# Optimization experiments

Measured on AMD Instinct MI355X. Metric: run time of the kernel, lower is better.

Reference implementation:

```python
import jax, jax.numpy as jnp
import numpy as np
import math

NL = 2
ENC = 64

def _ln(x, g, b):
    m = x.mean(-1, keepdims=True)
    v = ((x - m) ** 2).mean(-1, keepdims=True)
    return (x - m) * jax.lax.rsqrt(v + 1e-5) * g + b

def _sinu(vals):
    half = ENC // 2
    freq = jnp.exp(jnp.arange(half, dtype=vals.dtype) * (-math.log(10000.0) / half))
    a = vals[..., None] * freq
    return jnp.concatenate([jnp.sin(a), jnp.cos(a)], -1)

def _ssm(x, ng, nb, piw, pib, pw, pb, ig, ib):
    # SSMBlock with LinearAttention core: x + proj_out(LN(silu(z)*sigmoid(gate)))
    h = _ln(x, ng, nb)
    zi = h @ piw + pib
    z, gate = jnp.split(zi, 2, axis=-1)
    u = _ln(jax.nn.silu(z) * jax.nn.sigmoid(gate), ig, ib)
    return x + u @ pw + pb

def _fwd(s, attn_maps, km, se_w1, se_b1, se_w2, se_b2,
         f_ng, f_nb, f_piw, f_pib, f_pow, f_pob, f_ig, f_ib,
         b_ng, b_nb, b_piw, b_pib, b_pow, b_pob, b_ig, b_ib,
         mrg_w, mrg_b, nrm_g, nrm_b,
         ffn_ng, ffn_nb, ffn_w1, ffn_b1, ffn_w2, ffn_b2, H, W):
    B, K, D = s.shape
    w = attn_maps / (attn_maps.sum(-1, keepdims=True) + 1e-8)  # [B,K,N]
    gy = jnp.arange(H, dtype=s.dtype) / max(H - 1, 1)
    gx = jnp.arange(W, dtype=s.dtype) / max(W - 1, 1)
    grid_y = jnp.repeat(gy, W)  # [N], meshgrid-ij flattened
    grid_x = jnp.tile(gx, H)
    cy = (w * grid_y).sum(-1)  # [B,K]
    cx = (w * grid_x).sum(-1)
    spread = jnp.sqrt((w * ((grid_y - cy[..., None]) ** 2 + (grid_x - cx[..., None]) ** 2)).sum(-1))
    enc = jnp.concatenate([_sinu(cy), _sinu(cx), spread[..., None]], -1)  # [B,K,129]
    s = s + jax.nn.gelu(enc @ se_w1 + se_b1, approximate=False) @ se_w2 + se_b2
    # spatial order: identical every layer since attn_maps is fixed
    order = jnp.argsort(cy * W + cx, axis=-1)  # [B,K]
    rv = jnp.argsort(order, axis=-1)           # inverse permutation
    for i in range(NL):
        r = s
        so = jnp.take_along_axis(s, order[..., None], axis=1)
        f = _ssm(so, f_ng[i], f_nb[i], f_piw[i], f_pib[i], f_pow[i], f_pob[i], f_ig[i], f_ib[i])
        bb = jnp.flip(_ssm(jnp.flip(so, 1), b_ng[i], b_nb[i], b_piw[i], b_pib[i], b_pow[i], b_pob[i], b_ig[i], b_ib[i]), 1)
        m = jnp.concatenate([f, bb], -1) @ mrg_w[i] + mrg_b[i]
        s = _ln(r + jnp.take_along_axis(m, rv[..., None], axis=1), nrm_g[i], nrm_b[i])
        h = _ln(s, ffn_ng[i], ffn_nb[i])
        s = s + jax.nn.gelu(h @ ffn_w1[i] + ffn_b1[i], approximate=False) @ ffn_w2[i] + ffn_b2[i]
        s = s * km[..., None]
    return s

def setup_inputs() -> dict:
    B, K, D, DI, H, W = 32, 256, 512, 1024, 64, 64
    N = H * W
    ks = iter(jax.random.split(jax.random.key(0), 64))
    def g(shape, sc=0.02):
        return jax.random.normal(next(ks), shape, dtype=jnp.float32) * sc
    inp = {
        's': jax.random.normal(next(ks), (B, K, D), dtype=jnp.float32),
        'attn_maps': jax.random.uniform(next(ks), (B, K, N), dtype=jnp.float32),
        'km': jnp.ones((B, K), jnp.float32),
        'se_w1': g((2 * ENC + 1, D)), 'se_b1': jnp.zeros((D,), jnp.float32),
        'se_w2': g((D, D)), 'se_b2': jnp.zeros((D,), jnp.float32),
    }
    for p in ('f', 'b'):
        inp[p + '_ng'] = jnp.ones((NL, D), jnp.float32)
        inp[p + '_nb'] = jnp.zeros((NL, D), jnp.float32)
        inp[p + '_piw'] = g((NL, D, 2 * DI))
        inp[p + '_pib'] = jnp.zeros((NL, 2 * DI), jnp.float32)
        inp[p + '_pow'] = g((NL, DI, D))
        inp[p + '_pob'] = jnp.zeros((NL, D), jnp.float32)
        inp[p + '_ig'] = jnp.ones((NL, DI), jnp.float32)
        inp[p + '_ib'] = jnp.zeros((NL, DI), jnp.float32)
    inp['mrg_w'] = g((NL, 2 * D, D)); inp['mrg_b'] = jnp.zeros((NL, D), jnp.float32)
    inp['nrm_g'] = jnp.ones((NL, D), jnp.float32); inp['nrm_b'] = jnp.zeros((NL, D), jnp.float32)
    inp['ffn_ng'] = jnp.ones((NL, D), jnp.float32); inp['ffn_nb'] = jnp.zeros((NL, D), jnp.float32)
    inp['ffn_w1'] = g((NL, D, 4 * D)); inp['ffn_b1'] = jnp.zeros((NL, 4 * D), jnp.float32)
    inp['ffn_w2'] = g((NL, 4 * D, D)); inp['ffn_b2'] = jnp.zeros((NL, D), jnp.float32)
    inp['H'] = H
    inp['W'] = W
    return inp

def reference(s, attn_maps, km, se_w1, se_b1, se_w2, se_b2,
              f_ng, f_nb, f_piw, f_pib, f_pow, f_pob, f_ig, f_ib,
              b_ng, b_nb, b_piw, b_pib, b_pow, b_pob, b_ig, b_ib,
              mrg_w, mrg_b, nrm_g, nrm_b,
              ffn_ng, ffn_nb, ffn_w1, ffn_b1, ffn_w2, ffn_b2, H, W):
    return _fwd(s, attn_maps, km, se_w1, se_b1, se_w2, se_b2,
                f_ng, f_nb, f_piw, f_pib, f_pow, f_pob, f_ig, f_ib,
                b_ng, b_nb, b_piw, b_pib, b_pow, b_pob, b_ig, b_ib,
                mrg_w, mrg_b, nrm_g, nrm_b,
                ffn_ng, ffn_nb, ffn_w1, ffn_b1, ffn_w2, ffn_b2, H, W)
```

## Files before the change

### kernel.cpp

```cpp
#include <hip/hip_runtime.h>
#include <cstdint>
#include <cstddef>


typedef unsigned short u16;
typedef __bf16 bf16x8 __attribute__((ext_vector_type(8)));
typedef float f32x4 __attribute__((ext_vector_type(4)));

#define MROWS 8192

__device__ __forceinline__ u16 f2bf(float f){
  unsigned u = __float_as_uint(f);
  u += 0x7FFFu + ((u >> 16) & 1u);
  return (u16)(u >> 16);
}

__device__ __forceinline__ float wred64(float v){
#pragma unroll
  for (int o = 32; o > 0; o >>= 1) v += __shfl_xor(v, o, 64);
  return v;
}

#define GLD16(gp, lp) __builtin_amdgcn_global_load_lds( \
    (const __attribute__((address_space(1))) unsigned int*)(gp), \
    (__attribute__((address_space(3))) unsigned int*)(lp), 16, 0, 0)

__global__ __launch_bounds__(256) void transpose_w(
    const float* __restrict__ in, u16* __restrict__ out,
    int R, int C, int Kpad, int zgate){
  __shared__ float tile[32][33];
  int n0 = blockIdx.x << 5, k0 = blockIdx.y << 5;
  int tx = threadIdx.x & 31, ty = threadIdx.x >> 5;
#pragma unroll
  for (int i = 0; i < 32; i += 8){
    int k = k0 + ty + i, n = n0 + tx;
    int oc = n;
    if (zgate){ int g = n >> 5, sl = n & 31;
      oc = (sl < 16) ? (g << 4) + sl : (C >> 1) + (g << 4) + sl - 16; }
    tile[ty + i][tx] = (k < R) ? in[(size_t)k * C + oc] : 0.f;
  }
  __syncthreads();
#pragma unroll
  for (int i = 0; i < 32; i += 8){
    int n = n0 + ty + i, k = k0 + tx;
    out[(size_t)n * Kpad + k] = f2bf(tile[tx][ty + i]);
  }
}

__global__ __launch_bounds__(256) void perm_bias(
    const float* __restrict__ in, float* __restrict__ out){
  int n = blockIdx.x * 256 + threadIdx.x;
  int g = n >> 5, sl = n & 31;
  out[n] = in[(sl < 16) ? (g << 4) + sl : 1024 + (g << 4) + sl - 16];
}

__global__ __launch_bounds__(256) void stats_enc(
    const float* __restrict__ attn, u16* __restrict__ enc){
  int row = blockIdx.x;
  const float4* a4 = (const float4*)(attn + (size_t)row * 4096);
  int t = threadIdx.x;
  const float inv63 = 1.0f / 63.0f;
  float s0 = 0, sy = 0, sx = 0, sy2 = 0, sx2 = 0;
#pragma unroll
  for (int i = 0; i < 4; ++i){
    int c = t + 256 * i;
    float4 v = a4[c];
    int n = 4 * c;
#pragma unroll
    for (int e = 0; e < 4; ++e){
      float av = (&v.x)[e];
      int nn = n + e;
      float gy = (float)(nn >> 6) * inv63;
      float gx = (float)(nn & 63) * inv63;
      s0 += av; sy += av * gy; sx += av * gx;
      sy2 += av * gy * gy; sx2 += av * gx * gx;
    }
  }
  s0 = wred64(s0); sy = wred64(sy); sx = wred64(sx);
  sy2 = wred64(sy2); sx2 = wred64(sx2);
  __shared__ float red[4][5];
  __shared__ float outv[3];
  int wv = t >> 6, lane = t & 63;
  if (lane == 0){ red[wv][0]=s0; red[wv][1]=sy; red[wv][2]=sx; red[wv][3]=sy2; red[wv][4]=sx2; }
  __syncthreads();
  if (t == 0){
    float S=0, Ay=0, Ax=0, Ay2=0, Ax2=0;
    for (int w = 0; w < 4; ++w){ S+=red[w][0]; Ay+=red[w][1]; Ax+=red[w][2]; Ay2+=red[w][3]; Ax2+=red[w][4]; }
    float denom = S + 1e-8f;
    float cy = Ay / denom, cx = Ax / denom;
    float sp2 = (Ay2 - 2.f*cy*Ay + cy*cy*S + Ax2 - 2.f*cx*Ax + cx*cx*S) / denom;
    outv[0] = cy; outv[1] = cx; outv[2] = sqrtf(fmaxf(sp2, 0.f));
  }
  __syncthreads();
  if (t < 192){
    float cy = outv[0], cx = outv[1];
    float val = 0.f;
    if (t < 128){
      int j = t & 31;
      float fr = expf(-0.28782313662425572f * (float)j);
      float base = (t < 64) ? cy : cx;
      float ang = base * fr;
      val = ((t >> 5) & 1) ? cosf(ang) : sinf(ang);
    } else if (t == 128) val = outv[2];
    enc[(size_t)row * 192 + t] = f2bf(val);
  }
}

__global__ __launch_bounds__(256) void ln_dual(
    const float* __restrict__ x,
    const float* __restrict__ g1, const float* __restrict__ b1,
    const float* __restrict__ g2, const float* __restrict__ b2,
    u16* __restrict__ o1, u16* __restrict__ o2){
  int row = blockIdx.x * 4 + (threadIdx.x >> 6);
  int lane = threadIdx.x & 63, c = lane * 8;
  const float* xr = x + (size_t)row * 512 + c;
  float v[8];
  *(float4*)(v) = *(const float4*)(xr); *(float4*)(v+4) = *(const float4*)(xr+4);
  float s = 0.f;
#pragma unroll
  for (int j = 0; j < 8; ++j) s += v[j];
  float m = wred64(s) * (1.f/512.f);
  float q = 0.f;
#pragma unroll
  for (int j = 0; j < 8; ++j){ float d = v[j]-m; q += d*d; }
  float rstd = rsqrtf(wred64(q)*(1.f/512.f) + 1e-5f);
  float G1[8],B1[8],G2[8],B2[8];
  *(float4*)(G1)=*(const float4*)(g1+c); *(float4*)(G1+4)=*(const float4*)(g1+c+4);
  *(float4*)(B1)=*(const float4*)(b1+c); *(float4*)(B1+4)=*(const float4*)(b1+c+4);
  *(float4*)(G2)=*(const float4*)(g2+c); *(float4*)(G2+4)=*(const float4*)(g2+c+4);
  *(float4*)(B2)=*(const float4*)(b2+c); *(float4*)(B2+4)=*(const float4*)(b2+c+4);
  u16 u1[8] __attribute__((aligned(16)));
  u16 u2[8] __attribute__((aligned(16)));
#pragma unroll
  for (int j = 0; j < 8; ++j){
    float nv = (v[j]-m)*rstd;
    u1[j] = f2bf(nv*G1[j]+B1[j]);
    u2[j] = f2bf(nv*G2[j]+B2[j]);
  }
  *(uint4*)(o1 + (size_t)row*512 + c) = *(const uint4*)u1;
  *(uint4*)(o2 + (size_t)row*512 + c) = *(const uint4*)u2;
}

__global__ __launch_bounds__(256) void ln1024(
    const float* __restrict__ x, const float* __restrict__ g,
    const float* __restrict__ b, u16* __restrict__ o){
  int row = blockIdx.x * 4 + (threadIdx.x >> 6);
  int lane = threadIdx.x & 63, c = lane * 16;
  const float* xr = x + (size_t)row * 1024 + c;
  float v[16];
#pragma unroll
  for (int i = 0; i < 4; ++i) *(float4*)(v + 4*i) = *(const float4*)(xr + 4*i);
  float s = 0.f;
#pragma unroll
  for (int j = 0; j < 16; ++j) s += v[j];
  float m = wred64(s) * (1.f/1024.f);
  float q = 0.f;
#pragma unroll
  for (int j = 0; j < 16; ++j){ float d = v[j]-m; q += d*d; }
  float rstd = rsqrtf(wred64(q)*(1.f/1024.f) + 1e-5f);
  float G[16], B[16];
#pragma unroll
  for (int i = 0; i < 4; ++i){
    *(float4*)(G + 4*i) = *(const float4*)(g + c + 4*i);
    *(float4*)(B + 4*i) = *(const float4*)(b + c + 4*i);
  }
  u16 u[16] __attribute__((aligned(16)));
#pragma unroll
  for (int j = 0; j < 16; ++j) u[j] = f2bf((v[j]-m)*rstd*G[j] + B[j]);
  *(uint4*)(o + (size_t)row*1024 + c)     = *(const uint4*)(u);
  *(uint4*)(o + (size_t)row*1024 + c + 8) = *(const uint4*)(u + 8);
}

__global__ __launch_bounds__(256) void ln_double(
    const float* __restrict__ x,
    const float* __restrict__ ng, const float* __restrict__ nb,
    const float* __restrict__ fg, const float* __restrict__ fbv,
    float* __restrict__ s1, u16* __restrict__ h2){
  int row = blockIdx.x * 4 + (threadIdx.x >> 6);
  int lane = threadIdx.x & 63, c = lane * 8;
  const float* xr = x + (size_t)row * 512 + c;
  float v[8];
  *(float4*)(v) = *(const float4*)(xr); *(float4*)(v+4) = *(const float4*)(xr+4);
  float s = 0.f;
#pragma unroll
  for (int j = 0; j < 8; ++j) s += v[j];
  float m = wred64(s) * (1.f/512.f);
  float q = 0.f;
#pragma unroll
  for (int j = 0; j < 8; ++j){ float d = v[j]-m; q += d*d; }
  float rstd = rsqrtf(wred64(q)*(1.f/512.f) + 1e-5f);
  float NG[8],NB[8],FG[8],FB[8];
  *(float4*)(NG)=*(const float4*)(ng+c); *(float4*)(NG+4)=*(const float4*)(ng+c+4);
  *(float4*)(NB)=*(const float4*)(nb+c); *(float4*)(NB+4)=*(const float4*)(nb+c+4);
  *(float4*)(FG)=*(const float4*)(fg+c); *(float4*)(FG+4)=*(const float4*)(fg+c+4);
  *(float4*)(FB)=*(const float4*)(fbv+c);*(float4*)(FB+4)=*(const float4*)(fbv+c+4);
  float w[8];
#pragma unroll
  for (int j = 0; j < 8; ++j) w[j] = (v[j]-m)*rstd*NG[j] + NB[j];
  *(float4*)(s1 + (size_t)row*512 + c)   = *(const float4*)(w);
  *(float4*)(s1 + (size_t)row*512 + c+4) = *(const float4*)(w+4);
  float s2 = 0.f;
#pragma unroll
  for (int j = 0; j < 8; ++j) s2 += w[j];
  float m2 = wred64(s2) * (1.f/512.f);
  float q2 = 0.f;
#pragma unroll
  for (int j = 0; j < 8; ++j){ float d = w[j]-m2; q2 += d*d; }
  float rstd2 = rsqrtf(wred64(q2)*(1.f/512.f) + 1e-5f);
  u16 u[8] __attribute__((aligned(16)));
#pragma unroll
  for (int j = 0; j < 8; ++j) u[j] = f2bf((w[j]-m2)*rstd2*FG[j] + FB[j]);
  *(uint4*)(h2 + (size_t)row*512 + c) = *(const uint4*)u;
}

template<int EPI>
__global__ __launch_bounds__(256, 2) void gemm_bt(
    const u16* __restrict__ A, const u16* __restrict__ BT,
    const float* __restrict__ bias, const float* __restrict__ res,
    float* __restrict__ outF, u16* __restrict__ outB,
    const float* __restrict__ km,
    int K, int N, int ldo, int coloff){
  __shared__ u16 Asm[128 * 64];
  __shared__ u16 Bsm[128 * 64];
  const int tid = threadIdx.x, wv = tid >> 6, lane = tid & 63;
  const int m0 = blockIdx.y << 7, n0 = blockIdx.x << 7;
  const int wr = wv >> 1, wc = wv & 1;

  const int rload = (wv << 5) + (lane >> 3);
  const int ksrc = ((16 * (lane & 7)) ^ (((lane >> 3) & 7) << 4)) >> 1;
  const u16* gA = A + (size_t)(m0 + rload) * K + ksrc;
  const u16* gB = BT + (size_t)(n0 + rload) * K + ksrc;
  u16* ldsA = Asm + (wv << 11);
  u16* ldsB = Bsm + (wv << 11);

  f32x4 acc[4][4] = {};
  const int cbase = 16 * (lane >> 4);
  const int swz = (lane & 7) << 4;

  for (int kt = 0; kt < K; kt += 64){
#pragma unroll
    for (int it = 0; it < 4; ++it){
      GLD16(gA + (size_t)it * 8 * K + kt, ldsA + it * 512);
      GLD16(gB + (size_t)it * 8 * K + kt, ldsB + it * 512);
    }
    __syncthreads();
#pragma unroll
    for (int ks = 0; ks < 64; ks += 32){
      const int cs = ((2 * ks + cbase) ^ swz) >> 1;
      bf16x8 af[4], bfr[4];
#pragma unroll
      for (int m = 0; m < 4; ++m)
        af[m] = *reinterpret_cast<const bf16x8*>(&Asm[(wr*64 + m*16 + (lane & 15)) * 64 + cs]);
#pragma unroll
      for (int n = 0; n < 4; ++n)
        bfr[n] = *reinterpret_cast<const bf16x8*>(&Bsm[(wc*64 + n*16 + (lane & 15)) * 64 + cs]);
#pragma unroll
      for (int m = 0; m < 4; ++m)
#pragma unroll
        for (int n = 0; n < 4; ++n)
          acc[m][n] = __builtin_amdgcn_mfma_f32_16x16x32_bf16(af[m], bfr[n], acc[m][n], 0, 0, 0);
    }
    __syncthreads();
  }

  const int lr = (lane >> 4) << 2, lc = lane & 15;
#pragma unroll
  for (int m = 0; m < 4; ++m){
    const int grow0 = m0 + wr * 64 + m * 16 + lr;
    if constexpr (EPI == 3){
#pragma unroll
      for (int n = 0; n < 4; n += 2){
        const int zc = n0 + wc * 64 + n * 16 + lc;
        const float bz = bias[zc], bg = bias[zc + 16];
        const int ucol = ((n0 + wc * 64) >> 1) + (n << 3) + lc;
#pragma unroll
        for (int r = 0; r < 4; ++r){
          float z = acc[m][n][r] + bz;
          float g = acc[m][n + 1][r] + bg;
          outF[(size_t)(grow0 + r) * ldo + ucol] =
              (z / (1.f + expf(-z))) * (1.f / (1.f + expf(-g)));
        }
      }
    } else {
#pragma unroll
      for (int n = 0; n < 4; ++n){
        const int col = n0 + wc * 64 + n * 16 + lc;
        const float bv = bias[col];
#pragma unroll
        for (int r = 0; r < 4; ++r){
          const int grow = grow0 + r;
          float v = acc[m][n][r] + bv;
          if constexpr (EPI == 0){
            outB[(size_t)grow * ldo + col] = f2bf(0.5f * v * (1.f + erff(v * 0.70710678118654752f)));
          } else if constexpr (EPI == 1){
            outF[(size_t)grow * ldo + col] = v + res[(size_t)grow * N + col];
          } else if constexpr (EPI == 2){
            outF[(size_t)grow * ldo + col] = (v + res[(size_t)grow * N + col]) * km[grow];
          } else {
            outB[(size_t)grow * ldo + coloff + col] = f2bf(v + res[(size_t)grow * N + col]);
          }
        }
      }
    }
  }
}

extern "C" void kernel_launch(void* const* d_in, const int* in_sizes, int n_in,
                              void* d_out, int out_size, void* d_ws, size_t ws_size,
                              hipStream_t stream){
  (void)in_sizes; (void)n_in; (void)out_size; (void)ws_size;
  const float* s_in   = (const float*)d_in[0];
  const float* attn   = (const float*)d_in[1];
  const float* km     = (const float*)d_in[2];
  const float* se_w1  = (const float*)d_in[3];
  const float* se_b1  = (const float*)d_in[4];
  const float* se_w2  = (const float*)d_in[5];
  const float* se_b2  = (const float*)d_in[6];
  const float* png[2] = {(const float*)d_in[7],  (const float*)d_in[15]};
  const float* pnb[2] = {(const float*)d_in[8],  (const float*)d_in[16]};
  const float* ppiw[2]= {(const float*)d_in[9],  (const float*)d_in[17]};
  const float* ppib[2]= {(const float*)d_in[10], (const float*)d_in[18]};
  const float* ppow[2]= {(const float*)d_in[11], (const float*)d_in[19]};
  const float* ppob[2]= {(const float*)d_in[12], (const float*)d_in[20]};
  const float* pig[2] = {(const float*)d_in[13], (const float*)d_in[21]};
  const float* pibt[2]= {(const float*)d_in[14], (const float*)d_in[22]};
  const float* mrg_w  = (const float*)d_in[23];
  const float* mrg_b  = (const float*)d_in[24];
  const float* nrm_g  = (const float*)d_in[25];
  const float* nrm_b  = (const float*)d_in[26];
  const float* ffn_ng = (const float*)d_in[27];
  const float* ffn_nb = (const float*)d_in[28];
  const float* ffn_w1 = (const float*)d_in[29];
  const float* ffn_b1 = (const float*)d_in[30];
  const float* ffn_w2 = (const float*)d_in[31];
  const float* ffn_b2 = (const float*)d_in[32];
  float* out = (float*)d_out;

  char* ws = (char*)d_ws;
  size_t off = 0;
  auto alloc = [&](size_t bytes)->char*{
    char* p = ws + off; off += (bytes + 255) & ~(size_t)255; return p; };

  u16* w_sew1 = (u16*)alloc(512 * 192 * 2);
  u16* w_sew2 = (u16*)alloc(512 * 512 * 2);
  u16* w_piw[2][2]; u16* w_pow[2][2]; float* pibp[2][2];
  for (int d = 0; d < 2; ++d)
    for (int i = 0; i < 2; ++i){
      w_piw[d][i] = (u16*)alloc(2048 * 512 * 2);
      w_pow[d][i] = (u16*)alloc(512 * 1024 * 2);
      pibp[d][i]  = (float*)alloc(2048 * 4);
    }
  u16* w_mrg[2]; u16* w_ffn1[2]; u16* w_ffn2[2];
  for (int i = 0; i < 2; ++i){
    w_mrg[i]  = (u16*)alloc(512 * 1024 * 2);
    w_ffn1[i] = (u16*)alloc(2048 * 512 * 2);
    w_ffn2[i] = (u16*)alloc(512 * 2048 * 2);
  }
  u16*   enc  = (u16*)alloc((size_t)MROWS * 192 * 2);
  u16*   t1h2 = (u16*)alloc((size_t)MROWS * 512 * 2);
  float* sc   = (float*)alloc((size_t)MROWS * 512 * 4);
  u16*   hf   = (u16*)alloc((size_t)MROWS * 512 * 2);
  u16*   hb   = (u16*)alloc((size_t)MROWS * 512 * 2);
  char*  big  = alloc((size_t)MROWS * 1024 * 4);
  float* upre = (float*)big;
  float* r2   = (float*)big;
  u16*   t2   = (u16*)big;
  u16*   ubf  = (u16*)alloc((size_t)MROWS * 1024 * 2);
  u16*   fbuf = (u16*)alloc((size_t)MROWS * 1024 * 2);
  float* s1   = (float*)alloc((size_t)MROWS * 512 * 4);

  transpose_w<<<dim3(16, 6),  256, 0, stream>>>(se_w1, w_sew1, 129, 512, 192, 0);
  transpose_w<<<dim3(16, 16), 256, 0, stream>>>(se_w2, w_sew2, 512, 512, 512, 0);
  for (int d = 0; d < 2; ++d)
    for (int i = 0; i < 2; ++i){
      transpose_w<<<dim3(64, 16), 256, 0, stream>>>(ppiw[d] + (size_t)i*512*2048, w_piw[d][i], 512, 2048, 512, 1);
      transpose_w<<<dim3(16, 32), 256, 0, stream>>>(ppow[d] + (size_t)i*1024*512, w_pow[d][i], 1024, 512, 1024, 0);
      perm_bias<<<8, 256, 0, stream>>>(ppib[d] + (size_t)i*2048, pibp[d][i]);
    }
  for (int i = 0; i < 2; ++i){
    transpose_w<<<dim3(16, 32), 256, 0, stream>>>(mrg_w  + (size_t)i*1024*512, w_mrg[i],  1024, 512, 1024, 0);
    transpose_w<<<dim3(64, 16), 256, 0, stream>>>(ffn_w1 + (size_t)i*512*2048, w_ffn1[i], 512, 2048, 512, 0);
    transpose_w<<<dim3(16, 64), 256, 0, stream>>>(ffn_w2 + (size_t)i*2048*512, w_ffn2[i], 2048, 512, 2048, 0);
  }

  stats_enc<<<MROWS, 256, 0, stream>>>(attn, enc);
  gemm_bt<0><<<dim3(4, 64), 256, 0, stream>>>(enc,  w_sew1, se_b1, nullptr, nullptr, t1h2, nullptr, 192, 512, 512, 0);
  gemm_bt<1><<<dim3(4, 64), 256, 0, stream>>>(t1h2, w_sew2, se_b2, s_in,    sc,      nullptr, nullptr, 512, 512, 512, 0);

  for (int i = 0; i < 2; ++i){
    ln_dual<<<MROWS/4, 256, 0, stream>>>(sc, png[0]+i*512, pnb[0]+i*512,
                                         png[1]+i*512, pnb[1]+i*512, hf, hb);
    for (int d = 0; d < 2; ++d){
      const u16* h = d ? hb : hf;
      gemm_bt<3><<<dim3(16, 64), 256, 0, stream>>>(h, w_piw[d][i], pibp[d][i],
          nullptr, upre, nullptr, nullptr, 512, 2048, 1024, 0);
      ln1024<<<MROWS/4, 256, 0, stream>>>(upre, pig[d]+i*1024, pibt[d]+i*1024, ubf);
      gemm_bt<4><<<dim3(4, 64), 256, 0, stream>>>(ubf, w_pow[d][i], ppob[d]+i*512,
          sc, nullptr, fbuf, nullptr, 1024, 512, 1024, d*512);
    }
    gemm_bt<1><<<dim3(4, 64), 256, 0, stream>>>(fbuf, w_mrg[i], mrg_b+i*512,
        sc, r2, nullptr, nullptr, 1024, 512, 512, 0);
    ln_double<<<MROWS/4, 256, 0, stream>>>(r2, nrm_g+i*512, nrm_b+i*512,
        ffn_ng+i*512, ffn_nb+i*512, s1, t1h2);
    gemm_bt<0><<<dim3(16, 64), 256, 0, stream>>>(t1h2, w_ffn1[i], ffn_b1+i*2048,
        nullptr, nullptr, t2, nullptr, 512, 2048, 2048, 0);
    gemm_bt<2><<<dim3(4, 64), 256, 0, stream>>>(t2, w_ffn2[i], ffn_b2+i*512,
        s1, (i == 1 ? out : sc), nullptr, km, 2048, 512, 512, 0);
  }
}
```

Measured before the change: 927.9 us.

## Batch weight transposes, use BM=64 tiles for N=512 GEMMs, bf16 gate output

Merges all weight transposes into one launch driven by a descriptor table and drops the separate bias permutation kernel by indexing the bias directly in the epilogue. The GEMM gains a BM template parameter, and the N=512 GEMMs now use 64-row tiles, doubling their grid from 256 to 512 blocks to fill more compute units. The silu-gate epilogue now writes bf16 instead of fp32 and ln1024 reads bf16, halving that intermediate's traffic at some precision cost.

```diff
diff --git a/kernel.cpp b/kernel.cpp
--- a/kernel.cpp
+++ b/kernel.cpp
@@ -14,6 +14,9 @@
   u += 0x7FFFu + ((u >> 16) & 1u);
   return (u16)(u >> 16);
 }
+__device__ __forceinline__ float bf2f(u16 v){
+  return __uint_as_float((unsigned)v << 16);
+}
 
 __device__ __forceinline__ float wred64(float v){
 #pragma unroll
@@ -25,33 +28,34 @@
     (const __attribute__((address_space(1))) unsigned int*)(gp), \
     (__attribute__((address_space(3))) unsigned int*)(lp), 16, 0, 0)
 
-__global__ __launch_bounds__(256) void transpose_w(
-    const float* __restrict__ in, u16* __restrict__ out,
-    int R, int C, int Kpad, int zgate){
+struct TDesc { const float* src; u16* dst; int R, Kpad, C, zgate, nbx, base; };
+struct TPack { TDesc d[16]; };
+
+__global__ __launch_bounds__(256) void transpose_all(TPack p){
+  int bid = blockIdx.x;
+  TDesc dd = p.d[0];
+#pragma unroll
+  for (int i = 1; i < 16; ++i) if (bid >= p.d[i].base) dd = p.d[i];
+  int lb = bid - dd.base;
+  int bx = lb % dd.nbx, by = lb / dd.nbx;
+
   __shared__ float tile[32][33];
-  int n0 = blockIdx.x << 5, k0 = blockIdx.y << 5;
+  int n0 = bx << 5, k0 = by << 5;
   int tx = threadIdx.x & 31, ty = threadIdx.x >> 5;
 #pragma unroll
   for (int i = 0; i < 32; i += 8){
     int k = k0 + ty + i, n = n0 + tx;
     int oc = n;
-    if (zgate){ int g = n >> 5, sl = n & 31;
-      oc = (sl < 16) ? (g << 4) + sl : (C >> 1) + (g << 4) + sl - 16; }
-    tile[ty + i][tx] = (k < R) ? in[(size_t)k * C + oc] : 0.f;
+    if (dd.zgate){ int g = n >> 5, sl = n & 31;
+      oc = (sl < 16) ? (g << 4) + sl : (dd.C >> 1) + (g << 4) + sl - 16; }
+    tile[ty + i][tx] = (k < dd.R) ? dd.src[(size_t)k * dd.C + oc] : 0.f;
   }
   __syncthreads();
 #pragma unroll
   for (int i = 0; i < 32; i += 8){
     int n = n0 + ty + i, k = k0 + tx;
-    out[(size_t)n * Kpad + k] = f2bf(tile[tx][ty + i]);
-  }
-}
-
-__global__ __launch_bounds__(256) void perm_bias(
-    const float* __restrict__ in, float* __restrict__ out){
-  int n = blockIdx.x * 256 + threadIdx.x;
-  int g = n >> 5, sl = n & 31;
-  out[n] = in[(sl < 16) ? (g << 4) + sl : 1024 + (g << 4) + sl - 16];
+    dd.dst[(size_t)n * dd.Kpad + k] = f2bf(tile[tx][ty + i]);
+  }
 }
 
 __global__ __launch_bounds__(256) void stats_enc(
@@ -142,14 +146,17 @@
 }
 
 __global__ __launch_bounds__(256) void ln1024(
-    const float* __restrict__ x, const float* __restrict__ g,
+    const u16* __restrict__ x, const float* __restrict__ g,
     const float* __restrict__ b, u16* __restrict__ o){
   int row = blockIdx.x * 4 + (threadIdx.x >> 6);
   int lane = threadIdx.x & 63, c = lane * 16;
-  const float* xr = x + (size_t)row * 1024 + c;
+  const u16* xr = x + (size_t)row * 1024 + c;
+  u16 raw[16] __attribute__((aligned(16)));
+  *(uint4*)(raw)     = *(const uint4*)(xr);
+  *(uint4*)(raw + 8) = *(const uint4*)(xr + 8);
   float v[16];
 #pragma unroll
-  for (int i = 0; i < 4; ++i) *(float4*)(v + 4*i) = *(const float4*)(xr + 4*i);
+  for (int j = 0; j < 16; ++j) v[j] = bf2f(raw[j]);
   float s = 0.f;
 #pragma unroll
   for (int j = 0; j < 16; ++j) s += v[j];
@@ -213,49 +220,53 @@
   *(uint4*)(h2 + (size_t)row*512 + c) = *(const uint4*)u;
 }
 
-template<int EPI>
+template<int EPI, int BM>
 __global__ __launch_bounds__(256, 2) void gemm_bt(
     const u16* __restrict__ A, const u16* __restrict__ BT,
     const float* __restrict__ bias, const float* __restrict__ res,
     float* __restrict__ outF, u16* __restrict__ outB,
     const float* __restrict__ km,
     int K, int N, int ldo, int coloff){
-  __shared__ u16 Asm[128 * 64];
+  constexpr int MR = BM / 32;
+  __shared__ u16 Asm[BM * 64];
   __shared__ u16 Bsm[128 * 64];
   const int tid = threadIdx.x, wv = tid >> 6, lane = tid & 63;
-  const int m0 = blockIdx.y << 7, n0 = blockIdx.x << 7;
+  const int m0 = blockIdx.y * BM, n0 = blockIdx.x << 7;
   const int wr = wv >> 1, wc = wv & 1;
 
-  const int rload = (wv << 5) + (lane >> 3);
-  const int ksrc = ((16 * (lane & 7)) ^ (((lane >> 3) & 7) << 4)) >> 1;
-  const u16* gA = A + (size_t)(m0 + rload) * K + ksrc;
-  const u16* gB = BT + (size_t)(n0 + rload) * K + ksrc;
-  u16* ldsA = Asm + (wv << 11);
+  const int rowin = lane >> 3;
+  const int ksrc = ((16 * (lane & 7)) ^ (rowin << 4)) >> 1;
+  const int rA = wv * (BM / 4) + rowin;
+  const int rB = (wv << 5) + rowin;
+  const u16* gA = A + (size_t)(m0 + rA) * K + ksrc;
+  const u16* gB = BT + (size_t)(n0 + rB) * K + ksrc;
+  u16* ldsA = Asm + wv * (BM / 4) * 64;
   u16* ldsB = Bsm + (wv << 11);
 
-  f32x4 acc[4][4] = {};
+  f32x4 acc[MR][4] = {};
   const int cbase = 16 * (lane >> 4);
   const int swz = (lane & 7) << 4;
 
   for (int kt = 0; kt < K; kt += 64){
 #pragma unroll
-    for (int it = 0; it < 4; ++it){
+    for (int it = 0; it < BM / 32; ++it)
       GLD16(gA + (size_t)it * 8 * K + kt, ldsA + it * 512);
+#pragma unroll
+    for (int it = 0; it < 4; ++it)
       GLD16(gB + (size_t)it * 8 * K + kt, ldsB + it * 512);
-    }
     __syncthreads();
 #pragma unroll
     for (int ks = 0; ks < 64; ks += 32){
       const int cs = ((2 * ks + cbase) ^ swz) >> 1;
-      bf16x8 af[4], bfr[4];
-#pragma unroll
-      for (int m = 0; m < 4; ++m)
-        af[m] = *reinterpret_cast<const bf16x8*>(&Asm[(wr*64 + m*16 + (lane & 15)) * 64 + cs]);
+      bf16x8 af[MR], bfr[4];
+#pragma unroll
+      for (int m = 0; m < MR; ++m)
+        af[m] = *reinterpret_cast<const bf16x8*>(&Asm[(wr*(BM/2) + m*16 + (lane & 15)) * 64 + cs]);
 #pragma unroll
       for (int n = 0; n < 4; ++n)
         bfr[n] = *reinterpret_cast<const bf16x8*>(&Bsm[(wc*64 + n*16 + (lane & 15)) * 64 + cs]);
 #pragma unroll
-      for (int m = 0; m < 4; ++m)
+      for (int m = 0; m < MR; ++m)
 #pragma unroll
         for (int n = 0; n < 4; ++n)
           acc[m][n] = __builtin_amdgcn_mfma_f32_16x16x32_bf16(af[m], bfr[n], acc[m][n], 0, 0, 0);
@@ -265,20 +276,21 @@
 
   const int lr = (lane >> 4) << 2, lc = lane & 15;
 #pragma unroll
-  for (int m = 0; m < 4; ++m){
-    const int grow0 = m0 + wr * 64 + m * 16 + lr;
+  for (int m = 0; m < MR; ++m){
+    const int grow0 = m0 + wr * (BM/2) + m * 16 + lr;
     if constexpr (EPI == 3){
 #pragma unroll
       for (int n = 0; n < 4; n += 2){
         const int zc = n0 + wc * 64 + n * 16 + lc;
-        const float bz = bias[zc], bg = bias[zc + 16];
+        const int bi = ((zc >> 5) << 4) + lc;
+        const float bz = bias[bi], bg = bias[(N >> 1) + bi];
         const int ucol = ((n0 + wc * 64) >> 1) + (n << 3) + lc;
 #pragma unroll
         for (int r = 0; r < 4; ++r){
           float z = acc[m][n][r] + bz;
           float g = acc[m][n + 1][r] + bg;
-          outF[(size_t)(grow0 + r) * ldo + ucol] =
-              (z / (1.f + expf(-z))) * (1.f / (1.f + expf(-g)));
+          outB[(size_t)(grow0 + r) * ldo + ucol] =
+              f2bf((z / (1.f + expf(-z))) * (1.f / (1.f + expf(-g))));
         }
       }
     } else {
@@ -343,12 +355,11 @@
 
   u16* w_sew1 = (u16*)alloc(512 * 192 * 2);
   u16* w_sew2 = (u16*)alloc(512 * 512 * 2);
-  u16* w_piw[2][2]; u16* w_pow[2][2]; float* pibp[2][2];
+  u16* w_piw[2][2]; u16* w_pow[2][2];
   for (int d = 0; d < 2; ++d)
     for (int i = 0; i < 2; ++i){
       w_piw[d][i] = (u16*)alloc(2048 * 512 * 2);
       w_pow[d][i] = (u16*)alloc(512 * 1024 * 2);
-      pibp[d][i]  = (float*)alloc(2048 * 4);
     }
   u16* w_mrg[2]; u16* w_ffn1[2]; u16* w_ffn2[2];
   for (int i = 0; i < 2; ++i){
@@ -362,49 +373,56 @@
   u16*   hf   = (u16*)alloc((size_t)MROWS * 512 * 2);
   u16*   hb   = (u16*)alloc((size_t)MROWS * 512 * 2);
   char*  big  = alloc((size_t)MROWS * 1024 * 4);
-  float* upre = (float*)big;
+  u16*   upre = (u16*)big;
   float* r2   = (float*)big;
   u16*   t2   = (u16*)big;
   u16*   ubf  = (u16*)alloc((size_t)MROWS * 1024 * 2);
   u16*   fbuf = (u16*)alloc((size_t)MROWS * 1024 * 2);
   float* s1   = (float*)alloc((size_t)MROWS * 512 * 4);
 
-  transpose_w<<<dim3(16, 6),  256, 0, stream>>>(se_w1, w_sew1, 129, 512, 192, 0);
-  transpose_w<<<dim3(16, 16), 256, 0, stream>>>(se_w2, w_sew2, 512, 512, 512, 0);
+  TPack pk; int base = 0, di = 0;
+  auto push = [&](const float* src, u16* dst, int R, int Kpad, int C, int zg){
+    TDesc& t = pk.d[di++];
+    t.src = src; t.dst = dst; t.R = R; t.Kpad = Kpad; t.C = C; t.zgate = zg;
+    t.nbx = C / 32; t.base = base;
+    base += (C / 32) * (Kpad / 32);
+  };
+  push(se_w1, w_sew1, 129, 192, 512, 0);
+  push(se_w2, w_sew2, 512, 512, 512, 0);
   for (int d = 0; d < 2; ++d)
     for (int i = 0; i < 2; ++i){
-      transpose_w<<<dim3(64, 16), 256, 0, stream>>>(ppiw[d] + (size_t)i*512*2048, w_piw[d][i], 512, 2048, 512, 1);
-      transpose_w<<<dim3(16, 32), 256, 0, stream>>>(ppow[d] + (size_t)i*1024*512, w_pow[d][i], 1024, 512, 1024, 0);
-      perm_bias<<<8, 256, 0, stream>>>(ppib[d] + (size_t)i*2048, pibp[d][i]);
+      push(ppiw[d] + (size_t)i*512*2048, w_piw[d][i], 512, 512, 2048, 1);
+      push(ppow[d] + (size_t)i*1024*512, w_pow[d][i], 1024, 1024, 512, 0);
     }
   for (int i = 0; i < 2; ++i){
-    transpose_w<<<dim3(16, 32), 256, 0, stream>>>(mrg_w  + (size_t)i*1024*512, w_mrg[i],  1024, 512, 1024, 0);
-    transpose_w<<<dim3(64, 16), 256, 0, stream>>>(ffn_w1 + (size_t)i*512*2048, w_ffn1[i], 512, 2048, 512, 0);
-    transpose_w<<<dim3(16, 64), 256, 0, stream>>>(ffn_w2 + (size_t)i*2048*512, w_ffn2[i], 2048, 512, 2048, 0);
-  }
+    push(mrg_w  + (size_t)i*1024*512, w_mrg[i],  1024, 1024, 512, 0);
+    push(ffn_w1 + (size_t)i*512*2048, w_ffn1[i], 512, 512, 2048, 0);
+    push(ffn_w2 + (size_t)i*2048*512, w_ffn2[i], 2048, 2048, 512, 0);
+  }
+  transpose_all<<<base, 256, 0, stream>>>(pk);
 
   stats_enc<<<MROWS, 256, 0, stream>>>(attn, enc);
-  gemm_bt<0><<<dim3(4, 64), 256, 0, stream>>>(enc,  w_sew1, se_b1, nullptr, nullptr, t1h2, nullptr, 192, 512, 512, 0);
-  gemm_bt<1><<<dim3(4, 64), 256, 0, stream>>>(t1h2, w_sew2, se_b2, s_in,    sc,      nullptr, nullptr, 512, 512, 512, 0);
+  gemm_bt<0,64><<<dim3(4, 128), 256, 0, stream>>>(enc,  w_sew1, se_b1, nullptr, nullptr, t1h2, nullptr, 192, 512, 512, 0);
+  gemm_bt<1,64><<<dim3(4, 128), 256, 0, stream>>>(t1h2, w_sew2, se_b2, s_in,    sc,      nullptr, nullptr, 512, 512, 512, 0);
 
   for (int i = 0; i < 2; ++i){
     ln_dual<<<MROWS/4, 256, 0, stream>>>(sc, png[0]+i*512, pnb[0]+i*512,
                                          png[1]+i*512, pnb[1]+i*512, hf, hb);
     for (int d = 0; d < 2; ++d){
       const u16* h = d ? hb : hf;
-      gemm_bt<3><<<dim3(16, 64), 256, 0, stream>>>(h, w_piw[d][i], pibp[d][i],
-          nullptr, upre, nullptr, nullptr, 512, 2048, 1024, 0);
+      gemm_bt<3,128><<<dim3(16, 64), 256, 0, stream>>>(h, w_piw[d][i], ppib[d]+(size_t)i*2048,
+          nullptr, nullptr, upre, nullptr, 512, 2048, 1024, 0);
       ln1024<<<MROWS/4, 256, 0, stream>>>(upre, pig[d]+i*1024, pibt[d]+i*1024, ubf);
-      gemm_bt<4><<<dim3(4, 64), 256, 0, stream>>>(ubf, w_pow[d][i], ppob[d]+i*512,
+      gemm_bt<4,64><<<dim3(4, 128), 256, 0, stream>>>(ubf, w_pow[d][i], ppob[d]+i*512,
           sc, nullptr, fbuf, nullptr, 1024, 512, 1024, d*512);
     }
-    gemm_bt<1><<<dim3(4, 64), 256, 0, stream>>>(fbuf, w_mrg[i], mrg_b+i*512,
+    gemm_bt<1,64><<<dim3(4, 128), 256, 0, stream>>>(fbuf, w_mrg[i], mrg_b+i*512,
         sc, r2, nullptr, nullptr, 1024, 512, 512, 0);
     ln_double<<<MROWS/4, 256, 0, stream>>>(r2, nrm_g+i*512, nrm_b+i*512,
         ffn_ng+i*512, ffn_nb+i*512, s1, t1h2);
-    gemm_bt<0><<<dim3(16, 64), 256, 0, stream>>>(t1h2, w_ffn1[i], ffn_b1+i*2048,
+    gemm_bt<0,128><<<dim3(16, 64), 256, 0, stream>>>(t1h2, w_ffn1[i], ffn_b1+i*2048,
         nullptr, nullptr, t2, nullptr, 512, 2048, 2048, 0);
-    gemm_bt<2><<<dim3(4, 64), 256, 0, stream>>>(t2, w_ffn2[i], ffn_b2+i*512,
+    gemm_bt<2,64><<<dim3(4, 128), 256, 0, stream>>>(t2, w_ffn2[i], ffn_b2+i*512,
         s1, (i == 1 ? out : sc), nullptr, km, 2048, 512, 512, 0);
   }
 }
```

Result: faster. 832.2 us (-10.3%).
